# Performance work log

Measured on AMD Instinct MI355X. Metric: run time of the kernel, lower is better.

## Reference

```python
import jax, jax.numpy as jnp
import numpy as np

B, S, D = 8, 2048, 768
H = 4 * D  # MLP hidden
EPS = 1e-5


def setup_inputs() -> dict:
    key = jax.random.key(0)
    ks = jax.random.split(key, 12)
    sd = 1.0 / np.sqrt(D)
    sh = 1.0 / np.sqrt(H)
    return {
        "x": jax.random.normal(ks[0], (B, S, D), dtype=jnp.float32),
        "ln1_g": jnp.ones((D,), jnp.float32),
        "ln1_b": jnp.zeros((D,), jnp.float32),
        "ln2_g": jnp.ones((D,), jnp.float32),
        "ln2_b": jnp.zeros((D,), jnp.float32),
        "Wq": jax.random.normal(ks[1], (D, D), jnp.float32) * sd,
        "bq": jnp.zeros((D,), jnp.float32),
        "Wk": jax.random.normal(ks[2], (D, D), jnp.float32) * sd,
        "bk": jnp.zeros((D,), jnp.float32),
        "Wv": jax.random.normal(ks[3], (D, D), jnp.float32) * sd,
        "bv": jnp.zeros((D,), jnp.float32),
        "Wo": jax.random.normal(ks[4], (D, D), jnp.float32) * sd,
        "bo": jnp.zeros((D,), jnp.float32),
        "Wfc": jax.random.normal(ks[5], (D, H), jnp.float32) * sd,
        "bfc": jnp.zeros((H,), jnp.float32),
        "Wproj": jax.random.normal(ks[6], (H, D), jnp.float32) * sh,
        "bproj": jnp.zeros((D,), jnp.float32),
    }


def _layernorm(x, g, b):
    mu = jnp.mean(x, axis=-1, keepdims=True)
    var = jnp.mean(jnp.square(x - mu), axis=-1, keepdims=True)
    return (x - mu) * jax.lax.rsqrt(var + EPS) * g + b


def reference(x, ln1_g, ln1_b, ln2_g, ln2_b, Wq, bq, Wk, bk, Wv, bv, Wo, bo,
              Wfc, bfc, Wproj, bproj):
    d = x.shape[-1]
    # --- attention sub-block (single head, full D) ---
    h = _layernorm(x, ln1_g, ln1_b)
    q = h @ Wq + bq            # [B,S,D]
    k = h @ Wk + bk
    v = h @ Wv + bv
    scores = jnp.einsum("bsd,btd->bst", q, k) / jnp.sqrt(jnp.float32(d))
    attn = jax.nn.softmax(scores, axis=-1)  # softmax over keys (dim=2)
    y = jnp.einsum("bst,btd->bsd", attn, v)
    x = x + (y @ Wo + bo)
    # --- MLP sub-block (exact GELU like nn.GELU default) ---
    h2 = _layernorm(x, ln2_g, ln2_b)
    m = jax.nn.gelu(h2 @ Wfc + bfc, approximate=False)
    x = x + (m @ Wproj + bproj)  # dropout p=0 -> identity
    return x
```

## Files before the change

### kernel.cpp

```cpp
#include <hip/hip_runtime.h>
#include <hip/hip_bf16.h>

typedef __attribute__((ext_vector_type(8))) short short8;
typedef __attribute__((ext_vector_type(4))) float floatx4;

using bf16 = __hip_bfloat16;

__device__ __forceinline__ void cp16_g2l(bf16* lds_p, const bf16* g) {
  __builtin_amdgcn_global_load_lds(
      (const __attribute__((address_space(1))) unsigned int*)g,
      (__attribute__((address_space(3))) unsigned int*)lds_p,
      16, 0, 0);
}

__device__ __forceinline__ float gelu_exact(float x) {
  return 0.5f * x * (1.0f + erff(x * 0.70710678118654752f));
}

template<int MODE>
__global__ __launch_bounds__(256)
void gemm_bt(const bf16* __restrict__ A, long sAb, long lda,
             const bf16* __restrict__ Bt, long sBb, long ldb,
             const float* __restrict__ bias,
             const float* __restrict__ residf,
             const bf16* __restrict__ residb,
             void* __restrict__ out, long sOb,
             int N, int K, float scale)
{
  constexpr bool PA   = (MODE == 5);
  constexpr bool ONES = (MODE == 5);

  __shared__ __attribute__((aligned(16))) bf16 sA[2][128 * 32];
  __shared__ __attribute__((aligned(16))) bf16 sB[2][128 * 32];

  const int tid = threadIdx.x;
  const int l = tid & 63, w = tid >> 6;
  const int bz = blockIdx.z;
  const long row0 = (long)blockIdx.x * 128;
  const long col0 = (long)blockIdx.y * 128;

  const bf16* Ab = A + (long)bz * sAb;
  const bf16* Bb = Bt + (long)bz * sBb;

  const int sr = (w << 4) + (l >> 2);
  const int slot = (l & 3) ^ ((sr >> 1) & 3);
  const int kcd = (l & 3) << 3;
  const bf16* gA;
  long skipA, koA;
  if constexpr (PA) {
    gA    = Ab + ((long)(slot >> 1) * lda + row0 + sr) * 16 + ((slot & 1) << 3);
    skipA = 64 * 16;
    koA   = 32 * lda;
  } else {
    gA    = Ab + (row0 + sr) * lda + (slot << 3);
    skipA = 64 * lda;
    koA   = 32;
  }
  const bf16* gB = Bb + (col0 + sr) * ldb + (slot << 3);
  const long skipB = 64 * ldb;
  const int lofs = sr * 32 + kcd;

  floatx4 acc[4][4];
  #pragma unroll
  for (int i = 0; i < 4; ++i)
    #pragma unroll
    for (int j = 0; j < 4; ++j)
      acc[i][j] = (floatx4){0.f, 0.f, 0.f, 0.f};
  floatx4 accs[4];
  #pragma unroll
  for (int i = 0; i < 4; ++i) accs[i] = (floatx4){0.f, 0.f, 0.f, 0.f};
  const short8 b_ones = {0x3F80, 0x3F80, 0x3F80, 0x3F80,
                         0x3F80, 0x3F80, 0x3F80, 0x3F80};

  const int wr = (w >> 1) & 1, wc = w & 1;
  const int g = l >> 4, t = l & 15;
  const int swz = (g ^ ((t >> 1) & 3)) << 3;
  const int aoff = (wr * 64 + t) * 32 + swz;
  const int boff = (wc * 64 + t) * 32 + swz;

  const int nt = K >> 5;

  cp16_g2l(&sA[0][lofs],           gA);
  cp16_g2l(&sA[0][lofs] + 64 * 32, gA + skipA);
  cp16_g2l(&sB[0][lofs],           gB);
  cp16_g2l(&sB[0][lofs] + 64 * 32, gB + skipB);

  for (int kt = 0; kt < nt; ++kt) {
    const int cur = kt & 1;
    asm volatile("s_barrier" ::: "memory");
    if (kt + 1 < nt) {
      const long oA = (long)(kt + 1) * koA;
      const long oB = (long)(kt + 1) << 5;
      bf16* dA = &sA[cur ^ 1][lofs];
      bf16* dB = &sB[cur ^ 1][lofs];
      cp16_g2l(dA,           gA + oA);
      cp16_g2l(dA + 64 * 32, gA + oA + skipA);
      cp16_g2l(dB,           gB + oB);
      cp16_g2l(dB + 64 * 32, gB + oB + skipB);
      asm volatile("s_waitcnt vmcnt(4)" ::: "memory");
    } else {
      asm volatile("s_waitcnt vmcnt(0)" ::: "memory");
    }

    const bf16* cA = &sA[cur][0];
    const bf16* cB = &sB[cur][0];
    short8 a[4], b[4];
    #pragma unroll
    for (int m = 0; m < 4; ++m) a[m] = *(const short8*)(cA + aoff + m * 512);
    #pragma unroll
    for (int n = 0; n < 4; ++n) b[n] = *(const short8*)(cB + boff + n * 512);
    #pragma unroll
    for (int m = 0; m < 4; ++m)
      #pragma unroll
      for (int n = 0; n < 4; ++n)
        acc[m][n] = __builtin_amdgcn_mfma_f32_16x16x32_bf16(a[m], b[n], acc[m][n], 0, 0, 0);
    if constexpr (ONES) {
      #pragma unroll
      for (int m = 0; m < 4; ++m)
        accs[m] = __builtin_amdgcn_mfma_f32_16x16x32_bf16(a[m], b_ones, accs[m], 0, 0, 0);
    }
  }

  const long orow = row0 + wr * 64 + (g << 2);
  const long ocol = col0 + wc * 64 + t;

  if constexpr (MODE == 0 || MODE == 4) {
    bf16* O = (bf16*)out + (long)bz * sOb;
    float bv4[4];
    #pragma unroll
    for (int n = 0; n < 4; ++n) bv4[n] = bias[ocol + n * 16];
    #pragma unroll
    for (int m = 0; m < 4; ++m) {
      #pragma unroll
      for (int r = 0; r < 4; ++r) {
        bf16* Or = O + (orow + m * 16 + r) * (long)N + ocol;
        #pragma unroll
        for (int n = 0; n < 4; ++n) {
          float vv = acc[m][n][r] + bv4[n];
          if constexpr (MODE == 4) vv = gelu_exact(vv);
          Or[n * 16] = __float2bfloat16(vv);
        }
      }
    }
  } else if constexpr (MODE == 7) {
    bf16* O = (bf16*)out;
    float bv4[4];
    #pragma unroll
    for (int n = 0; n < 4; ++n) bv4[n] = bias[ocol + n * 16];
    #pragma unroll
    for (int m = 0; m < 4; ++m) {
      #pragma unroll
      for (int r = 0; r < 4; ++r) {
        const long rb = (orow + m * 16 + r) * (long)N + ocol;
        #pragma unroll
        for (int n = 0; n < 4; ++n)
          O[rb + n * 16] =
              __float2bfloat16(acc[m][n][r] + bv4[n] + residf[rb + n * 16]);
      }
    }
  } else if constexpr (MODE == 8) {
    float* O = (float*)out;
    float bv4[4];
    #pragma unroll
    for (int n = 0; n < 4; ++n) bv4[n] = bias[ocol + n * 16];
    #pragma unroll
    for (int m = 0; m < 4; ++m) {
      #pragma unroll
      for (int r = 0; r < 4; ++r) {
        const long rb = (orow + m * 16 + r) * (long)N + ocol;
        #pragma unroll
        for (int n = 0; n < 4; ++n)
          O[rb + n * 16] = acc[m][n][r] + bv4[n] +
                           __bfloat162float(residb[rb + n * 16]);
      }
    }
  } else if constexpr (MODE == 5) {
    bf16* O = (bf16*)out + (long)bz * sOb;
    #pragma unroll
    for (int m = 0; m < 4; ++m) {
      #pragma unroll
      for (int r = 0; r < 4; ++r) {
        const long rr = orow + m * 16 + r;
        const float inv = 1.0f / accs[m][r];
        bf16* Or = O + rr * (long)N + ocol;
        #pragma unroll
        for (int n = 0; n < 4; ++n)
          Or[n * 16] = __float2bfloat16(acc[m][n][r] * inv);
      }
    }
  } else {
    bf16* O = (bf16*)out + (long)bz * sOb;
    const long pb = (col0 >> 4) + wc * 4;
    #pragma unroll
    for (int n = 0; n < 4; ++n) {
      bf16* Opan = O + (pb + n) * ((long)N * 16) + t;
      #pragma unroll
      for (int m = 0; m < 4; ++m) {
        #pragma unroll
        for (int r = 0; r < 4; ++r)
          Opan[(orow + m * 16 + r) * 16] =
              __float2bfloat16(__expf(acc[m][n][r] * scale));
      }
    }
  }
}

__global__ __launch_bounds__(256)
void ln_kernel(const float* __restrict__ X, const float* __restrict__ G,
               const float* __restrict__ Bv, bf16* __restrict__ H)
{
  const int tid = threadIdx.x;
  const long row = blockIdx.x;
  const float* xr = X + row * 768;
  const float v0 = xr[tid], v1 = xr[tid + 256], v2 = xr[tid + 512];
  float s = v0 + v1 + v2;
  float s2 = v0 * v0 + v1 * v1 + v2 * v2;
  #pragma unroll
  for (int o = 32; o > 0; o >>= 1) {
    s += __shfl_xor(s, o);
    s2 += __shfl_xor(s2, o);
  }
  __shared__ float red[8];
  const int w = tid >> 6, l = tid & 63;
  if (l == 0) { red[w] = s; red[w + 4] = s2; }
  __syncthreads();
  s = red[0] + red[1] + red[2] + red[3];
  s2 = red[4] + red[5] + red[6] + red[7];
  const float mu = s * (1.f / 768.f);
  const float var = s2 * (1.f / 768.f) - mu * mu;
  const float rstd = rsqrtf(var + 1e-5f);
  bf16* hr = H + row * 768;
  hr[tid]       = __float2bfloat16((v0 - mu) * rstd * G[tid]       + Bv[tid]);
  hr[tid + 256] = __float2bfloat16((v1 - mu) * rstd * G[tid + 256] + Bv[tid + 256]);
  hr[tid + 512] = __float2bfloat16((v2 - mu) * rstd * G[tid + 512] + Bv[tid + 512]);
}

__global__ __launch_bounds__(256)
void lnb_kernel(const bf16* __restrict__ X, const float* __restrict__ G,
                const float* __restrict__ Bv, bf16* __restrict__ H)
{
  const int tid = threadIdx.x;
  const long row = blockIdx.x;
  const bf16* xr = X + row * 768;
  const float v0 = __bfloat162float(xr[tid]);
  const float v1 = __bfloat162float(xr[tid + 256]);
  const float v2 = __bfloat162float(xr[tid + 512]);
  float s = v0 + v1 + v2;
  float s2 = v0 * v0 + v1 * v1 + v2 * v2;
  #pragma unroll
  for (int o = 32; o > 0; o >>= 1) {
    s += __shfl_xor(s, o);
    s2 += __shfl_xor(s2, o);
  }
  __shared__ float red[8];
  const int w = tid >> 6, l = tid & 63;
  if (l == 0) { red[w] = s; red[w + 4] = s2; }
  __syncthreads();
  s = red[0] + red[1] + red[2] + red[3];
  s2 = red[4] + red[5] + red[6] + red[7];
  const float mu = s * (1.f / 768.f);
  const float var = s2 * (1.f / 768.f) - mu * mu;
  const float rstd = rsqrtf(var + 1e-5f);
  bf16* hr = H + row * 768;
  hr[tid]       = __float2bfloat16((v0 - mu) * rstd * G[tid]       + Bv[tid]);
  hr[tid + 256] = __float2bfloat16((v1 - mu) * rstd * G[tid + 256] + Bv[tid + 256]);
  hr[tid + 512] = __float2bfloat16((v2 - mu) * rstd * G[tid + 512] + Bv[tid + 512]);
}

__global__ void transpose_w(const float* __restrict__ W, bf16* __restrict__ Wt,
                            int K, int N)
{
  __shared__ float tile[32][33];
  const int n0 = blockIdx.x * 32, k0 = blockIdx.y * 32;
  const int tx = threadIdx.x, ty = threadIdx.y;
  #pragma unroll
  for (int j = ty; j < 32; j += 8)
    tile[j][tx] = W[(long)(k0 + j) * N + n0 + tx];
  __syncthreads();
  #pragma unroll
  for (int j = ty; j < 32; j += 8)
    Wt[(long)(n0 + j) * K + k0 + tx] = __float2bfloat16(tile[tx][j]);
}

__global__ void transpose_v(const bf16* __restrict__ QKV, bf16* __restrict__ Vt)
{
  __shared__ bf16 tile[32][33];
  const int d0 = blockIdx.x * 32, s0 = blockIdx.y * 32, b = blockIdx.z;
  const int tx = threadIdx.x, ty = threadIdx.y;
  #pragma unroll
  for (int j = ty; j < 32; j += 8)
    tile[j][tx] = QKV[((long)b * 2048 + s0 + j) * 2304 + 1536 + d0 + tx];
  __syncthreads();
  #pragma unroll
  for (int j = ty; j < 32; j += 8)
    Vt[(long)b * 768 * 2048 + (long)(d0 + j) * 2048 + s0 + tx] = tile[tx][j];
}

__global__ void concat3(const float* __restrict__ a, const float* __restrict__ b,
                        const float* __restrict__ c, float* __restrict__ o)
{
  const int i = threadIdx.x + blockIdx.x * 256;
  if (i < 768) { o[i] = a[i]; o[i + 768] = b[i]; o[i + 1536] = c[i]; }
}

extern "C" void kernel_launch(void* const* d_in, const int* in_sizes, int n_in,
                              void* d_out, int out_size, void* d_ws, size_t ws_size,
                              hipStream_t stream)
{
  const float* x     = (const float*)d_in[0];
  const float* ln1g  = (const float*)d_in[1];
  const float* ln1b  = (const float*)d_in[2];
  const float* ln2g  = (const float*)d_in[3];
  const float* ln2b  = (const float*)d_in[4];
  const float* Wq    = (const float*)d_in[5];
  const float* bq    = (const float*)d_in[6];
  const float* Wk    = (const float*)d_in[7];
  const float* bk    = (const float*)d_in[8];
  const float* Wv    = (const float*)d_in[9];
  const float* bvv   = (const float*)d_in[10];
  const float* Wo    = (const float*)d_in[11];
  const float* bo    = (const float*)d_in[12];
  const float* Wfc   = (const float*)d_in[13];
  const float* bfc   = (const float*)d_in[14];
  const float* Wproj = (const float*)d_in[15];
  const float* bproj = (const float*)d_in[16];
  float* out = (float*)d_out;

  constexpr int Bz = 8, S = 2048, D = 768, Hh = 3072, QKVN = 3 * D;
  constexpr long Mtot = (long)Bz * S;

  char* ws = (char*)d_ws;
  size_t off = 0;
  auto alloc = [&](size_t bytes) -> char* {
    char* p = ws + off;
    off += (bytes + 255) & ~(size_t)255;
    return p;
  };
  bf16* wqkvT = (bf16*)alloc((size_t)QKVN * D * 2);
  bf16* woT   = (bf16*)alloc((size_t)D * D * 2);
  bf16* wfcT  = (bf16*)alloc((size_t)Hh * D * 2);
  bf16* wprT  = (bf16*)alloc((size_t)D * Hh * 2);
  float* bqkv = (float*)alloc((size_t)QKVN * 4);
  bf16* hb    = (bf16*)alloc((size_t)Mtot * D * 2);
  bf16* qkv   = (bf16*)alloc((size_t)Mtot * QKVN * 2);
  bf16* vtb   = (bf16*)alloc((size_t)Mtot * D * 2);
  bf16* yb    = (bf16*)alloc((size_t)Mtot * D * 2);
  bf16* x1b = qkv;

  int nbat = Bz;
  size_t region = (size_t)nbat * S * S * 2;
  const size_t mbytes = (size_t)Mtot * Hh * 2;
  if (region < mbytes) region = mbytes;
  if (off + region > ws_size) {
    nbat = 1;
    region = mbytes;
  }
  char* reg = alloc(region);
  bf16* attn = (bf16*)reg;
  bf16* mb = (bf16*)reg;

  const dim3 tb(32, 8);

  transpose_w<<<dim3(D / 32, D / 32), tb, 0, stream>>>(Wq, wqkvT, D, D);
  transpose_w<<<dim3(D / 32, D / 32), tb, 0, stream>>>(Wk, wqkvT + (size_t)D * D, D, D);
  transpose_w<<<dim3(D / 32, D / 32), tb, 0, stream>>>(Wv, wqkvT + 2 * (size_t)D * D, D, D);
  transpose_w<<<dim3(D / 32, D / 32), tb, 0, stream>>>(Wo, woT, D, D);
  transpose_w<<<dim3(Hh / 32, D / 32), tb, 0, stream>>>(Wfc, wfcT, D, Hh);
  transpose_w<<<dim3(D / 32, Hh / 32), tb, 0, stream>>>(Wproj, wprT, Hh, D);
  concat3<<<3, 256, 0, stream>>>(bq, bk, bvv, bqkv);

  ln_kernel<<<(int)Mtot, 256, 0, stream>>>(x, ln1g, ln1b, hb);

  gemm_bt<0><<<dim3(Mtot / 128, QKVN / 128, 1), 256, 0, stream>>>(
      hb, 0, D, wqkvT, 0, D, bqkv, nullptr, nullptr, qkv, 0, QKVN, D, 1.f);
  transpose_v<<<dim3(D / 32, S / 32, Bz), tb, 0, stream>>>(qkv, vtb);

  const float sc = 0.03608439182435161f;
  for (int g0 = 0; g0 < Bz; g0 += nbat) {
    const bf16* qg  = qkv + (long)g0 * S * QKVN;
    const bf16* kg  = qkv + (long)g0 * S * QKVN + D;
    const bf16* vtg = vtb + (long)g0 * D * S;
    bf16* yg = yb + (long)g0 * S * D;
    gemm_bt<6><<<dim3(S / 128, S / 128, nbat), 256, 0, stream>>>(
        qg, (long)S * QKVN, QKVN, kg, (long)S * QKVN, QKVN, nullptr, nullptr,
        nullptr, attn, (long)S * S, S, D, sc);
    gemm_bt<5><<<dim3(S / 128, D / 128, nbat), 256, 0, stream>>>(
        attn, (long)S * S, S, vtg, (long)D * S, S, nullptr, nullptr,
        nullptr, yg, (long)S * D, D, S, 1.f);
  }

  gemm_bt<7><<<dim3(Mtot / 128, D / 128, 1), 256, 0, stream>>>(
      yb, 0, D, woT, 0, D, bo, x, nullptr, x1b, 0, D, D, 1.f);

  lnb_kernel<<<(int)Mtot, 256, 0, stream>>>(x1b, ln2g, ln2b, hb);

  gemm_bt<4><<<dim3(Mtot / 128, Hh / 128, 1), 256, 0, stream>>>(
      hb, 0, D, wfcT, 0, D, bfc, nullptr, nullptr, mb, 0, Hh, D, 1.f);
  gemm_bt<8><<<dim3(Mtot / 128, D / 128, 1), 256, 0, stream>>>(
      mb, 0, Hh, wprT, 0, Hh, bproj, nullptr, x1b, out, 0, D, Hh, 1.f);
}
```

Before: 566.2 us.

## Shrink GEMM tiles to 64x64 with single-wavefront blocks

Measured after the change: 834.1 us. 1.47x slower.

```diff
diff --git a/kernel.cpp b/kernel.cpp
--- a/kernel.cpp
+++ b/kernel.cpp
@@ -18,7 +18,7 @@
 }
 
 template<int MODE>
-__global__ __launch_bounds__(256)
+__global__ __launch_bounds__(64)
 void gemm_bt(const bf16* __restrict__ A, long sAb, long lda,
              const bf16* __restrict__ Bt, long sBb, long ldb,
              const float* __restrict__ bias,
@@ -30,35 +30,31 @@
   constexpr bool PA   = (MODE == 5);
   constexpr bool ONES = (MODE == 5);
 
-  __shared__ __attribute__((aligned(16))) bf16 sA[2][128 * 32];
-  __shared__ __attribute__((aligned(16))) bf16 sB[2][128 * 32];
-
-  const int tid = threadIdx.x;
-  const int l = tid & 63, w = tid >> 6;
+  __shared__ __attribute__((aligned(16))) bf16 sA[2][64 * 32];
+  __shared__ __attribute__((aligned(16))) bf16 sB[2][64 * 32];
+
+  const int l = threadIdx.x;
   const int bz = blockIdx.z;
-  const long row0 = (long)blockIdx.x * 128;
-  const long col0 = (long)blockIdx.y * 128;
+  const long row0 = (long)blockIdx.x * 64;
+  const long col0 = (long)blockIdx.y * 64;
 
   const bf16* Ab = A + (long)bz * sAb;
   const bf16* Bb = Bt + (long)bz * sBb;
 
-  const int sr = (w << 4) + (l >> 2);
-  const int slot = (l & 3) ^ ((sr >> 1) & 3);
-  const int kcd = (l & 3) << 3;
-  const bf16* gA;
-  long skipA, koA;
-  if constexpr (PA) {
-    gA    = Ab + ((long)(slot >> 1) * lda + row0 + sr) * 16 + ((slot & 1) << 3);
-    skipA = 64 * 16;
-    koA   = 32 * lda;
-  } else {
-    gA    = Ab + (row0 + sr) * lda + (slot << 3);
-    skipA = 64 * lda;
-    koA   = 32;
-  }
-  const bf16* gB = Bb + (col0 + sr) * ldb + (slot << 3);
-  const long skipB = 64 * ldb;
-  const int lofs = sr * 32 + kcd;
+  long offA[4], offB[4];
+  #pragma unroll
+  for (int j = 0; j < 4; ++j) {
+    const int L = l + j * 64;
+    const int r = L >> 2;
+    const int us = (L & 3) ^ ((r >> 1) & 3);
+    if constexpr (PA) {
+      offA[j] = (long)(us >> 1) * lda * 16 + (row0 + r) * 16 + ((us & 1) << 3);
+    } else {
+      offA[j] = (row0 + r) * lda + (us << 3);
+    }
+    offB[j] = (col0 + r) * ldb + (us << 3);
+  }
+  const long koA = PA ? 32 * lda : 32;
 
   floatx4 acc[4][4];
   #pragma unroll
@@ -72,32 +68,38 @@
   const short8 b_ones = {0x3F80, 0x3F80, 0x3F80, 0x3F80,
                          0x3F80, 0x3F80, 0x3F80, 0x3F80};
 
-  const int wr = (w >> 1) & 1, wc = w & 1;
   const int g = l >> 4, t = l & 15;
   const int swz = (g ^ ((t >> 1) & 3)) << 3;
-  const int aoff = (wr * 64 + t) * 32 + swz;
-  const int boff = (wc * 64 + t) * 32 + swz;
+  int aoff[4], boff[4];
+  #pragma unroll
+  for (int m = 0; m < 4; ++m) {
+    aoff[m] = (m * 16 + t) * 32 + swz;
+    boff[m] = (m * 16 + t) * 32 + swz;
+  }
 
   const int nt = K >> 5;
 
-  cp16_g2l(&sA[0][lofs],           gA);
-  cp16_g2l(&sA[0][lofs] + 64 * 32, gA + skipA);
-  cp16_g2l(&sB[0][lofs],           gB);
-  cp16_g2l(&sB[0][lofs] + 64 * 32, gB + skipB);
+  #pragma unroll
+  for (int j = 0; j < 4; ++j)
+    cp16_g2l(&sA[0][(l + j * 64) * 8], Ab + offA[j]);
+  #pragma unroll
+  for (int j = 0; j < 4; ++j)
+    cp16_g2l(&sB[0][(l + j * 64) * 8], Bb + offB[j]);
 
   for (int kt = 0; kt < nt; ++kt) {
     const int cur = kt & 1;
-    asm volatile("s_barrier" ::: "memory");
     if (kt + 1 < nt) {
       const long oA = (long)(kt + 1) * koA;
       const long oB = (long)(kt + 1) << 5;
-      bf16* dA = &sA[cur ^ 1][lofs];
-      bf16* dB = &sB[cur ^ 1][lofs];
-      cp16_g2l(dA,           gA + oA);
-      cp16_g2l(dA + 64 * 32, gA + oA + skipA);
-      cp16_g2l(dB,           gB + oB);
-      cp16_g2l(dB + 64 * 32, gB + oB + skipB);
-      asm volatile("s_waitcnt vmcnt(4)" ::: "memory");
+      bf16* dA = &sA[cur ^ 1][0];
+      bf16* dB = &sB[cur ^ 1][0];
+      #pragma unroll
+      for (int j = 0; j < 4; ++j)
+        cp16_g2l(dA + (l + j * 64) * 8, Ab + oA + offA[j]);
+      #pragma unroll
+      for (int j = 0; j < 4; ++j)
+        cp16_g2l(dB + (l + j * 64) * 8, Bb + oB + offB[j]);
+      asm volatile("s_waitcnt vmcnt(8)" ::: "memory");
     } else {
       asm volatile("s_waitcnt vmcnt(0)" ::: "memory");
     }
@@ -106,9 +108,9 @@
     const bf16* cB = &sB[cur][0];
     short8 a[4], b[4];
     #pragma unroll
-    for (int m = 0; m < 4; ++m) a[m] = *(const short8*)(cA + aoff + m * 512);
-    #pragma unroll
-    for (int n = 0; n < 4; ++n) b[n] = *(const short8*)(cB + boff + n * 512);
+    for (int m = 0; m < 4; ++m) a[m] = *(const short8*)(cA + aoff[m]);
+    #pragma unroll
+    for (int n = 0; n < 4; ++n) b[n] = *(const short8*)(cB + boff[n]);
     #pragma unroll
     for (int m = 0; m < 4; ++m)
       #pragma unroll
@@ -121,8 +123,8 @@
     }
   }
 
-  const long orow = row0 + wr * 64 + (g << 2);
-  const long ocol = col0 + wc * 64 + t;
+  const long orow = row0 + (g << 2);
+  const long ocol = col0 + t;
 
   if constexpr (MODE == 0 || MODE == 4) {
     bf16* O = (bf16*)out + (long)bz * sOb;
@@ -190,7 +192,7 @@
     }
   } else {
     bf16* O = (bf16*)out + (long)bz * sOb;
-    const long pb = (col0 >> 4) + wc * 4;
+    const long pb = col0 >> 4;
     #pragma unroll
     for (int n = 0; n < 4; ++n) {
       bf16* Opan = O + (pb + n) * ((long)N * 16) + t;
@@ -371,7 +373,7 @@
 
   ln_kernel<<<(int)Mtot, 256, 0, stream>>>(x, ln1g, ln1b, hb);
 
-  gemm_bt<0><<<dim3(Mtot / 128, QKVN / 128, 1), 256, 0, stream>>>(
+  gemm_bt<0><<<dim3(Mtot / 64, QKVN / 64, 1), 64, 0, stream>>>(
       hb, 0, D, wqkvT, 0, D, bqkv, nullptr, nullptr, qkv, 0, QKVN, D, 1.f);
   transpose_v<<<dim3(D / 32, S / 32, Bz), tb, 0, stream>>>(qkv, vtb);
 
@@ -381,21 +383,21 @@
     const bf16* kg  = qkv + (long)g0 * S * QKVN + D;
     const bf16* vtg = vtb + (long)g0 * D * S;
     bf16* yg = yb + (long)g0 * S * D;
-    gemm_bt<6><<<dim3(S / 128, S / 128, nbat), 256, 0, stream>>>(
+    gemm_bt<6><<<dim3(S / 64, S / 64, nbat), 64, 0, stream>>>(
         qg, (long)S * QKVN, QKVN, kg, (long)S * QKVN, QKVN, nullptr, nullptr,
         nullptr, attn, (long)S * S, S, D, sc);
-    gemm_bt<5><<<dim3(S / 128, D / 128, nbat), 256, 0, stream>>>(
+    gemm_bt<5><<<dim3(S / 64, D / 64, nbat), 64, 0, stream>>>(
         attn, (long)S * S, S, vtg, (long)D * S, S, nullptr, nullptr,
         nullptr, yg, (long)S * D, D, S, 1.f);
   }
 
-  gemm_bt<7><<<dim3(Mtot / 128, D / 128, 1), 256, 0, stream>>>(
+  gemm_bt<7><<<dim3(Mtot / 64, D / 64, 1), 64, 0, stream>>>(
       yb, 0, D, woT, 0, D, bo, x, nullptr, x1b, 0, D, D, 1.f);
 
   lnb_kernel<<<(int)Mtot, 256, 0, stream>>>(x1b, ln2g, ln2b, hb);
 
-  gemm_bt<4><<<dim3(Mtot / 128, Hh / 128, 1), 256, 0, stream>>>(
+  gemm_bt<4><<<dim3(Mtot / 64, Hh / 64, 1), 64, 0, stream>>>(
       hb, 0, D, wfcT, 0, D, bfc, nullptr, nullptr, mb, 0, Hh, D, 1.f);
-  gemm_bt<8><<<dim3(Mtot / 128, D / 128, 1), 256, 0, stream>>>(
+  gemm_bt<8><<<dim3(Mtot / 64, D / 64, 1), 64, 0, stream>>>(
       mb, 0, Hh, wprT, 0, Hh, bproj, nullptr, x1b, out, 0, D, Hh, 1.f);
 }
```
